# Kernel tuning notes

Hardware: AMD Instinct MI355X
Metric: run time of the kernel (lower is better)

The kernel has to match this reference:

```python
import jax, jax.numpy as jnp
import numpy as np

N = 50000      # nodes
E = 800000     # edges
D_IN, D_HID, D_OUT = 1433, 64, 7
EPS = 1e-7       # eps[float32] in hgcn Hyperboloid
MIN_NORM = 1e-15
MAX_NORM = 1e6
# c = 1 -> K = 1/c = 1, sqrtK = 1 (folded into constants below)


def proj(x):
    # reset time coordinate so point lies on the hyperboloid
    y = x[:, 1:]
    y_sqnorm = jnp.sum(y * y, axis=1, keepdims=True)
    x0 = jnp.sqrt(jnp.clip(1.0 + y_sqnorm, EPS))
    return jnp.concatenate([x0, y], axis=1)


def proj_tan0(u):
    return jnp.concatenate([jnp.zeros_like(u[:, :1]), u[:, 1:]], axis=1)


def expmap0(u):
    x = u[:, 1:]
    x_norm = jnp.clip(jnp.linalg.norm(x, axis=1, keepdims=True), MIN_NORM)
    theta = x_norm
    res = jnp.concatenate([jnp.cosh(theta), jnp.sinh(theta) * x / x_norm], axis=1)
    return proj(res)


def logmap0(x):
    y = x[:, 1:]
    y_norm = jnp.clip(jnp.linalg.norm(y, axis=1, keepdims=True), MIN_NORM)
    theta = jnp.clip(x[:, :1], 1.0 + EPS)
    return jnp.concatenate([jnp.zeros_like(theta), jnp.arccosh(theta) * y / y_norm], axis=1)


def minkowski_dot(x, y):
    return jnp.sum(x * y, axis=-1, keepdims=True) - 2.0 * x[:, :1] * y[:, :1]


def proj_tan(u, x):
    ux = jnp.sum(x[:, 1:] * u[:, 1:], axis=1, keepdims=True)
    v0 = ux / jnp.clip(x[:, :1], EPS)
    return jnp.concatenate([v0, u[:, 1:]], axis=1)


def expmap(u, x):
    normu = jnp.sqrt(jnp.clip(minkowski_dot(u, u), EPS))
    normu = jnp.minimum(normu, MAX_NORM)
    theta = jnp.clip(normu, MIN_NORM)
    result = jnp.cosh(theta) * x + jnp.sinh(theta) * u / theta
    return proj(result)


def ptransp0(x, u):
    x0, y = x[:, :1], x[:, 1:]
    y_norm = jnp.clip(jnp.linalg.norm(y, axis=1, keepdims=True), MIN_NORM)
    yn = y / y_norm
    v = jnp.concatenate([-y_norm, (1.0 - x0) * yn], axis=1)
    alpha = jnp.sum(yn * u[:, 1:], axis=1, keepdims=True)
    return proj_tan(u - alpha * v, x)


def mobius_add(x, y):
    u = logmap0(y)
    v = ptransp0(x, u)
    return expmap(v, x)


def hyp_linear(x, W, b):
    # mobius_matvec then hyperbolic bias add (dropout=0)
    mv = expmap0(logmap0(x) @ W.T)
    res = proj(mv)
    hyp_bias = proj(expmap0(proj_tan0(b[None, :])))
    return proj(mobius_add(res, hyp_bias))


def hyp_agg(x, row, col, edge_weight):
    # spmm(adj, logmap0(x)) via edge-list scatter-add
    xt = logmap0(x)
    msg = edge_weight[:, None] * xt[col]          # [E, d]
    support = jax.ops.segment_sum(msg, row, num_segments=N)
    return proj(expmap0(support))


def hyp_act(x):
    xt = jax.nn.relu(logmap0(x))
    xt = proj_tan0(xt)
    return proj(expmap0(xt))


def setup_inputs() -> dict:
    key = jax.random.key(0)
    ks = jax.random.split(key, 8)
    return {
        "x": jax.random.normal(ks[0], (N, D_IN), dtype=jnp.float32),
        "row": jax.random.randint(ks[1], (E,), 0, N),
        "col": jax.random.randint(ks[2], (E,), 0, N),
        "edge_weight": jax.random.uniform(ks[3], (E,), dtype=jnp.float32) * 0.1,
        "W1": jax.random.normal(ks[4], (D_HID, D_IN), dtype=jnp.float32) * 0.02,
        "b1": jax.random.normal(ks[5], (D_HID,), dtype=jnp.float32) * 0.02,
        "W2": jax.random.normal(ks[6], (D_OUT, D_HID), dtype=jnp.float32) * 0.05,
        "b2": jax.random.normal(ks[7], (D_OUT,), dtype=jnp.float32) * 0.02,
    }


def reference(x, row, col, edge_weight, W1, b1, W2, b2):
    # map features to the hyperboloid
    x_hyp = proj(expmap0(proj_tan0(x)))
    # layer 1: HypLinear -> HypAgg -> HypAct
    h = hyp_act(hyp_agg(hyp_linear(x_hyp, W1, b1), row, col, edge_weight))
    # layer 2
    h = hyp_act(hyp_agg(hyp_linear(h, W2, b2), row, col, edge_weight))
    # back to tangent space at origin
    return proj_tan0(logmap0(h))
```

## Files before the change

kernel.cpp:

```cpp
#include <hip/hip_runtime.h>
#include <hip/hip_bf16.h>

#define NN 50000
#define EE 800000
#define DIN 1433
#define KTOT 1432
#define KHALF 716
#define NKT 23
#define NB 196
#define EPSC 1e-7f
#define MINN 1e-15f
#define MAXN 1e6f

typedef __attribute__((ext_vector_type(8))) short bf16x8;
typedef __attribute__((ext_vector_type(4))) float f32x4;

#define WF_OFF     0
#define Z1A_OFF    94208
#define Z1B_OFF    (Z1A_OFF + 3200000)
#define XTB_OFF    (Z1B_OFF + 3200000)
#define XT3_OFF    (XTB_OFF + 1600000)
#define CNT_OFF    (XT3_OFF + 400000)
#define ROWPTR_OFF (CNT_OFF + 50000)
#define CUR_OFF    (ROWPTR_OFF + 50002)
#define BSUM_OFF   (CUR_OFF + 50000)
#define UB_OFF     (BSUM_OFF + 256)
#define EP_OFF     (UB_OFF + 128)

__device__ __forceinline__ float wsum(float v) {
#pragma unroll
  for (int o = 1; o < 64; o <<= 1) v += __shfl_xor(v, o, 64);
  return v;
}

__device__ __forceinline__ float gsum8(float v) {
#pragma unroll
  for (int o = 1; o < 8; o <<= 1) v += __shfl_xor(v, o, 64);
  return v;
}

__device__ __forceinline__ void split_bf(float v, unsigned int& hbits16, unsigned int& lbits16) {
  unsigned int b = __float_as_uint(v);
  unsigned int hb = b & 0xFFFF0000u;
  float r = v - __uint_as_float(hb);
  unsigned int lb = __float_as_uint(r);
  lbits16 = (lb + 0x7FFFu + ((lb >> 16) & 1u)) >> 16;
  hbits16 = hb >> 16;
}

__device__ __forceinline__ unsigned short f2bf_rne(float v) {
  unsigned int b = __float_as_uint(v);
  return (unsigned short)((b + 0x7FFFu + ((b >> 16) & 1u)) >> 16);
}
__device__ __forceinline__ float bf2f(unsigned short u) {
  return __uint_as_float(((unsigned int)u) << 16);
}

__device__ __forceinline__ float fsinh(float x) {
  float e = __expf(x);
  return 0.5f * (e - __fdividef(1.f, e));
}
__device__ __forceinline__ float facoshp(float z) {
  return __logf(z + sqrtf(fmaxf(z * z - 1.f, 0.f)));
}

__device__ float bias_tangent(const float* b, int lane, int D) {
  const bool sp = (lane >= 1) && (lane < D);
  float bsp = sp ? b[lane] : 0.f;
  float rb = fmaxf(sqrtf(wsum(bsp * bsp)), MINN);
  float bsh = fsinh(rb);
  float hb = sp ? bsh * __fdividef(bsp, rb) : 0.f;
  float hbn2 = wsum(hb * hb);
  float hb0 = sqrtf(fmaxf(1.f + hbn2, EPSC));
  float hbyn = fmaxf(sqrtf(hbn2), MINN);
  return sp ? facoshp(fmaxf(hb0, 1.f + EPSC)) * __fdividef(hb, hbyn) : 0.f;
}

__device__ float chain_with_u(float z, float u, int lane, int D) {
  const bool sp = (lane >= 1) && (lane < D);
  float s = sp ? z : 0.f;
  float r = fmaxf(sqrtf(wsum(s * s)), MINN);
  float sh = fsinh(r);
  float y = sp ? sh * __fdividef(s, r) : 0.f;
  float yn2 = wsum(y * y);
  float x0 = sqrtf(fmaxf(1.f + yn2, EPSC));
  float y_norm = fmaxf(sqrtf(yn2), MINN);
  float ynv = sp ? __fdividef(y, y_norm) : 0.f;
  float alpha = wsum(ynv * u);
  float wsp = sp ? u - alpha * (1.f - x0) * ynv : 0.f;
  float ux = wsum(y * wsp);
  float v0 = __fdividef(ux, fmaxf(x0, EPSC));
  float vt = (lane == 0) ? v0 : wsp;
  float md = wsum(vt * vt) - 2.f * v0 * v0;
  float nu = sqrtf(fmaxf(md, EPSC));
  nu = fminf(nu, MAXN);
  float th = fmaxf(nu, MINN);
  float e = __expf(th), ei = __fdividef(1.f, e);
  float cth = 0.5f * (e + ei), sth = 0.5f * (e - ei);
  float resx = (lane == 0) ? x0 : y;
  float eres = fmaf(cth, resx, sth * __fdividef(vt, th));
  float en2 = wsum(sp ? eres * eres : 0.f);
  float e0 = sqrtf(fmaxf(1.f + en2, EPSC));
  float eyn = fmaxf(sqrtf(en2), MINN);
  return sp ? facoshp(fmaxf(e0, 1.f + EPSC)) * __fdividef(eres, eyn) : 0.f;
}

__device__ float agg_act_chain(float sin_, int lane, int D) {
  const bool sp = (lane >= 1) && (lane < D);
  float s = sp ? sin_ : 0.f;
  float r = fmaxf(sqrtf(wsum(s * s)), MINN);
  float sh = fsinh(r);
  float g = sp ? sh * __fdividef(s, r) : 0.f;
  float gn2 = wsum(g * g);
  float g0 = sqrtf(fmaxf(1.f + gn2, EPSC));
  float gyn = fmaxf(sqrtf(gn2), MINN);
  float l = sp ? facoshp(fmaxf(g0, 1.f + EPSC)) * __fdividef(g, gyn) : 0.f;
  float t = fmaxf(l, 0.f);
  float rt = fmaxf(sqrtf(wsum(t * t)), MINN);
  float sht = fsinh(rt);
  float h = sp ? sht * __fdividef(t, rt) : 0.f;
  float hn2 = wsum(h * h);
  float h0 = sqrtf(fmaxf(1.f + hn2, EPSC));
  float hyn = fmaxf(sqrtf(hn2), MINN);
  return sp ? facoshp(fmaxf(h0, 1.f + EPSC)) * __fdividef(h, hyn) : 0.f;
}

__device__ float agg_act_chain8(float sin_, int f) {
  const bool sp = (f >= 1) && (f < 7);
  float s = sp ? sin_ : 0.f;
  float r = fmaxf(sqrtf(gsum8(s * s)), MINN);
  float sh = fsinh(r);
  float g = sp ? sh * __fdividef(s, r) : 0.f;
  float gn2 = gsum8(g * g);
  float g0 = sqrtf(fmaxf(1.f + gn2, EPSC));
  float gyn = fmaxf(sqrtf(gn2), MINN);
  float l = sp ? facoshp(fmaxf(g0, 1.f + EPSC)) * __fdividef(g, gyn) : 0.f;
  float t = fmaxf(l, 0.f);
  float rt = fmaxf(sqrtf(gsum8(t * t)), MINN);
  float sht = fsinh(rt);
  float h = sp ? sht * __fdividef(t, rt) : 0.f;
  float hn2 = gsum8(h * h);
  float h0 = sqrtf(fmaxf(1.f + hn2, EPSC));
  float hyn = fmaxf(sqrtf(hn2), MINN);
  return sp ? facoshp(fmaxf(h0, 1.f + EPSC)) * __fdividef(h, hyn) : 0.f;
}

__global__ __launch_bounds__(256) void prep_wb_zero(const float* __restrict__ W1,
                                                    const float* __restrict__ b1,
                                                    const float* __restrict__ b2,
                                                    unsigned short* __restrict__ wfrag,
                                                    float* __restrict__ ub,
                                                    int* __restrict__ cnt) {
  if (blockIdx.x >= 93) {
    int i = (blockIdx.x - 93) * 256 + threadIdx.x;
    if (i < NN) cnt[i] = 0;
    return;
  }
  if (blockIdx.x == 92) {
    const int w = threadIdx.x >> 6, lane = threadIdx.x & 63;
    if (w == 0) ub[lane] = bias_tangent(b1, lane, 64);
    else if (w == 1) ub[64 + lane] = bias_tangent(b2, lane, 7);
    return;
  }
  int idx = blockIdx.x * 256 + threadIdx.x;
  int lane = idx & 63;
  int c = (idx >> 6) & 7;
  int rest = idx >> 9;
  int kt = rest % NKT;
  int half = rest / NKT;
  int type = c >> 2, nt = c & 3;
  int col = nt * 16 + (lane & 15);
  unsigned short vals[8];
#pragma unroll
  for (int i = 0; i < 8; ++i) {
    int lk = kt * 32 + (lane >> 4) * 8 + i;
    float wv = (lk < KHALF) ? W1[col * DIN + half * KHALF + lk + 1] : 0.f;
    unsigned int h16, l16;
    split_bf(wv, h16, l16);
    vals[i] = (unsigned short)((type == 0) ? h16 : l16);
  }
  unsigned short* dst = wfrag + (((size_t)(half * NKT + kt) * 8 + c) * 64 + lane) * 8;
#pragma unroll
  for (int i = 0; i < 8; ++i) dst[i] = vals[i];
}

__global__ __launch_bounds__(256) void k_blocksum(const int* __restrict__ cnt,
                                                  int* __restrict__ bsum) {
  __shared__ int wpart[4];
  int i = blockIdx.x * 256 + threadIdx.x;
  int v = (i < NN) ? cnt[i] : 0;
  int s = v;
#pragma unroll
  for (int o = 1; o < 64; o <<= 1) s += __shfl_xor(s, o, 64);
  if ((threadIdx.x & 63) == 0) wpart[threadIdx.x >> 6] = s;
  __syncthreads();
  if (threadIdx.x == 0) bsum[blockIdx.x] = wpart[0] + wpart[1] + wpart[2] + wpart[3];
}

__global__ __launch_bounds__(256) void k_scan_apply(const int* __restrict__ cnt,
                                                    const int* __restrict__ bsum,
                                                    int* __restrict__ rowptr,
                                                    int* __restrict__ cur) {
  __shared__ int s[256];
  __shared__ int base_sh;
  const int t = threadIdx.x;
  const int b = blockIdx.x;
  int bv = (t < NB) ? bsum[t] : 0;
  s[t] = bv;
  __syncthreads();
  for (int o = 1; o < 256; o <<= 1) {
    int a = (t >= o) ? s[t - o] : 0;
    __syncthreads();
    s[t] += a;
    __syncthreads();
  }
  if (t == b) base_sh = s[b] - bv;
  __syncthreads();
  const int base = base_sh;
  __syncthreads();
  int i = b * 256 + t;
  int v = (i < NN) ? cnt[i] : 0;
  s[t] = v;
  __syncthreads();
  for (int o = 1; o < 256; o <<= 1) {
    int a = (t >= o) ? s[t - o] : 0;
    __syncthreads();
    s[t] += a;
    __syncthreads();
  }
  int ex = s[t] - v + base;
  if (i < NN) { rowptr[i] = ex; cur[i] = ex; }
  if (i == NN - 1) rowptr[NN] = EE;
}

__global__ __launch_bounds__(256) void gemm_hist(const float* __restrict__ x,
                                                 const unsigned short* __restrict__ wfrag,
                                                 float* __restrict__ z,
                                                 const int* __restrict__ row,
                                                 int* __restrict__ cnt) {
  if (blockIdx.y == 2) {
    int e = blockIdx.x * 512 + threadIdx.x;
    if (e < EE) atomicAdd(&cnt[row[e]], 1);
    e += 256;
    if (e < EE) atomicAdd(&cnt[row[e]], 1);
    return;
  }
  __shared__ __align__(16) float XA[3 * 1024];
  __shared__ __align__(16) unsigned short BB[2][8][64][8];
  const int tid = threadIdx.x;
  const int w = tid >> 6, lane = tid & 63;
  const int row0 = blockIdx.x * 32;
  const int half = blockIdx.y;
  const unsigned short* wf = wfrag + (size_t)half * NKT * 4096;
  float* zp = z + (size_t)half * 3200000;
  const int nt0 = (w >> 1) * 2;

  auto stageB = [&](int kt, int p) {
    const unsigned short* src = wf + (size_t)kt * 4096 + (2 * w) * 512 + lane * 8;
    __builtin_amdgcn_global_load_lds(
        (const __attribute__((address_space(1))) unsigned int*)src,
        (__attribute__((address_space(3))) unsigned int*)(&BB[p][2 * w][0][0]), 16, 0, 0);
    __builtin_amdgcn_global_load_lds(
        (const __attribute__((address_space(1))) unsigned int*)(src + 512),
        (__attribute__((address_space(3))) unsigned int*)(&BB[p][2 * w + 1][0][0]), 16, 0, 0);
  };
  auto stageA = [&](int kt, int q) {
    const int r = w * 8 + (lane >> 3);
    const int lb = (lane & 7) ^ (r & 7);
    int grow = row0 + r; if (grow >= NN) grow = NN - 1;
    size_t off = (size_t)grow * DIN + 1 + half * KHALF + kt * 32 + lb * 4;
    if (off > (size_t)NN * DIN - 4) off = (size_t)NN * DIN - 4;
    __builtin_amdgcn_global_load_lds(
        (const __attribute__((address_space(1))) unsigned int*)(x + off),
        (__attribute__((address_space(3))) unsigned int*)(XA + q * 1024 + w * 256),
        16, 0, 0);
  };

  f32x4 acc[2];
  acc[0] = (f32x4){0.f, 0.f, 0.f, 0.f};
  acc[1] = (f32x4){0.f, 0.f, 0.f, 0.f};

  stageB(0, 0);
  stageA(0, 0);
  stageA(1, 1);
  __builtin_amdgcn_sched_barrier(0);
  asm volatile("s_waitcnt vmcnt(1)" ::: "memory");
  __builtin_amdgcn_s_barrier();
  __builtin_amdgcn_sched_barrier(0);

  const int rr = (w & 1) * 16 + (lane & 15);
  const int b0 = (lane >> 4) * 2;
  const int pb0 = (b0 ^ (rr & 7)) * 4;
  const int pb1 = ((b0 + 1) ^ (rr & 7)) * 4;

  for (int kt = 0; kt < NKT; ++kt) {
    if (kt + 1 < NKT) stageB(kt + 1, (kt + 1) & 1);
    if (kt + 2 < NKT) stageA(kt + 2, (kt + 2) % 3);
    const float* xa = XA + (kt % 3) * 1024 + rr * 32;
    float4 f0 = *(const float4*)(xa + pb0);
    float4 f1 = *(const float4*)(xa + pb1);
    float af[8] = {f0.x, f0.y, f0.z, f0.w, f1.x, f1.y, f1.z, f1.w};
    unsigned int h[8], l[8];
#pragma unroll
    for (int j = 0; j < 8; ++j) split_bf(af[j], h[j], l[j]);
    bf16x8 ah, al;
#pragma unroll
    for (int j = 0; j < 8; ++j) { ah[j] = (short)h[j]; al[j] = (short)l[j]; }
    bf16x8 bh[2], bl[2];
#pragma unroll
    for (int n = 0; n < 2; ++n) {
      bh[n] = *(const bf16x8*)&BB[kt & 1][nt0 + n][lane][0];
      bl[n] = *(const bf16x8*)&BB[kt & 1][4 + nt0 + n][lane][0];
    }
    __builtin_amdgcn_s_setprio(1);
#pragma unroll
    for (int n = 0; n < 2; ++n) {
      acc[n] = __builtin_amdgcn_mfma_f32_16x16x32_bf16(ah, bh[n], acc[n], 0, 0, 0);
      acc[n] = __builtin_amdgcn_mfma_f32_16x16x32_bf16(ah, bl[n], acc[n], 0, 0, 0);
      acc[n] = __builtin_amdgcn_mfma_f32_16x16x32_bf16(al, bh[n], acc[n], 0, 0, 0);
    }
    __builtin_amdgcn_s_setprio(0);
    if (kt + 1 < NKT) {
      __builtin_amdgcn_sched_barrier(0);
      asm volatile("s_waitcnt lgkmcnt(0)" ::: "memory");
      if (kt + 2 < NKT) asm volatile("s_waitcnt vmcnt(1)" ::: "memory");
      else              asm volatile("s_waitcnt vmcnt(0)" ::: "memory");
      __builtin_amdgcn_s_barrier();
      __builtin_amdgcn_sched_barrier(0);
    }
  }
#pragma unroll
  for (int n = 0; n < 2; ++n)
#pragma unroll
    for (int i = 0; i < 4; ++i) {
      int orow = row0 + (w & 1) * 16 + (lane >> 4) * 4 + i;
      int ocol = (nt0 + n) * 16 + (lane & 15);
      if (orow < NN) zp[(size_t)orow * 64 + ocol] = acc[n][i];
    }
}

__global__ __launch_bounds__(256) void node1_scatter(const float* __restrict__ z1a,
                                                     const float* __restrict__ z1b,
                                                     const float* __restrict__ ub,
                                                     unsigned short* __restrict__ xtb,
                                                     const int* __restrict__ row,
                                                     const int* __restrict__ col,
                                                     const float* __restrict__ ew,
                                                     int* __restrict__ cur,
                                                     uint2* __restrict__ ep) {
  if (blockIdx.x >= 12500) {
    int e = (blockIdx.x - 12500) * 256 + threadIdx.x;
    if (e < EE) {
      int p = atomicAdd(&cur[row[e]], 1);
      uint2 q;
      q.x = (unsigned int)col[e];
      q.y = __float_as_uint(ew[e]);
      ep[p] = q;
    }
    return;
  }
  const int node = blockIdx.x * 4 + (threadIdx.x >> 6);
  const int lane = threadIdx.x & 63;
  const int idx = node * 64 + lane;
  float z = z1a[idx] + z1b[idx];
  float u1 = ub[lane];
  float o = chain_with_u(z, u1, lane, 64);
  xtb[idx] = f2bf_rne(o);
}

__global__ __launch_bounds__(256) void agg1_node2(const int* __restrict__ rowptr,
                                                  const uint2* __restrict__ ep,
                                                  const unsigned short* __restrict__ xtb,
                                                  const float* __restrict__ W2,
                                                  const float* __restrict__ ub,
                                                  float* __restrict__ xt3) {
  const int node = blockIdx.x * 4 + (threadIdx.x >> 6);
  const int lane = threadIdx.x & 63;
  const int s0 = rowptr[node], s1 = rowptr[node + 1];
  float a0 = 0.f, a1 = 0.f, a2 = 0.f, a3 = 0.f;
  float a4 = 0.f, a5 = 0.f, a6 = 0.f, a7 = 0.f;
  for (int p = s0; p < s1; p += 8) {
    int p1 = min(p + 1, s1 - 1), p2 = min(p + 2, s1 - 1), p3 = min(p + 3, s1 - 1);
    int p4 = min(p + 4, s1 - 1), p5 = min(p + 5, s1 - 1), p6 = min(p + 6, s1 - 1), p7 = min(p + 7, s1 - 1);
    uint2 q0 = ep[p], q1 = ep[p1], q2 = ep[p2], q3 = ep[p3];
    uint2 q4 = ep[p4], q5 = ep[p5], q6 = ep[p6], q7 = ep[p7];
    float w0 = __uint_as_float(q0.y);
    float w1 = (p + 1 < s1) ? __uint_as_float(q1.y) : 0.f;
    float w2 = (p + 2 < s1) ? __uint_as_float(q2.y) : 0.f;
    float w3 = (p + 3 < s1) ? __uint_as_float(q3.y) : 0.f;
    float w4 = (p + 4 < s1) ? __uint_as_float(q4.y) : 0.f;
    float w5 = (p + 5 < s1) ? __uint_as_float(q5.y) : 0.f;
    float w6 = (p + 6 < s1) ? __uint_as_float(q6.y) : 0.f;
    float w7 = (p + 7 < s1) ? __uint_as_float(q7.y) : 0.f;
    a0 = fmaf(w0, bf2f(xtb[(size_t)q0.x * 64 + lane]), a0);
    a1 = fmaf(w1, bf2f(xtb[(size_t)q1.x * 64 + lane]), a1);
    a2 = fmaf(w2, bf2f(xtb[(size_t)q2.x * 64 + lane]), a2);
    a3 = fmaf(w3, bf2f(xtb[(size_t)q3.x * 64 + lane]), a3);
    a4 = fmaf(w4, bf2f(xtb[(size_t)q4.x * 64 + lane]), a4);
    a5 = fmaf(w5, bf2f(xtb[(size_t)q5.x * 64 + lane]), a5);
    a6 = fmaf(w6, bf2f(xtb[(size_t)q6.x * 64 + lane]), a6);
    a7 = fmaf(w7, bf2f(xtb[(size_t)q7.x * 64 + lane]), a7);
  }
  float acc = ((a0 + a1) + (a2 + a3)) + ((a4 + a5) + (a6 + a7));
  float xt2 = agg_act_chain(acc, lane, 64);
  float z2 = 0.f;
#pragma unroll
  for (int jj = 1; jj < 7; ++jj) {
    float wv = W2[jj * 64 + lane];
    float sjj = wsum(xt2 * wv);
    if (lane == jj) z2 = sjj;
  }
  float u2 = ub[64 + lane];
  float o = chain_with_u(z2, u2, lane, 7);
  if (lane < 8) xt3[node * 8 + lane] = o;
}

__global__ __launch_bounds__(256) void agg2_final(const int* __restrict__ rowptr,
                                                  const uint2* __restrict__ ep,
                                                  const float* __restrict__ xt3,
                                                  float* __restrict__ out) {
  const int node = blockIdx.x * 32 + (threadIdx.x >> 3);
  const int f = threadIdx.x & 7;
  const int nc = (node < NN) ? node : (NN - 1);
  const int s0 = rowptr[nc], s1 = rowptr[nc + 1];
  float a0 = 0.f, a1 = 0.f, a2 = 0.f, a3 = 0.f;
  for (int p = s0; p < s1; p += 4) {
    int p1 = min(p + 1, s1 - 1), p2 = min(p + 2, s1 - 1), p3 = min(p + 3, s1 - 1);
    uint2 q0 = ep[p], q1 = ep[p1], q2 = ep[p2], q3 = ep[p3];
    float w0 = __uint_as_float(q0.y);
    float w1 = (p + 1 < s1) ? __uint_as_float(q1.y) : 0.f;
    float w2 = (p + 2 < s1) ? __uint_as_float(q2.y) : 0.f;
    float w3 = (p + 3 < s1) ? __uint_as_float(q3.y) : 0.f;
    a0 = fmaf(w0, xt3[(size_t)q0.x * 8 + f], a0);
    a1 = fmaf(w1, xt3[(size_t)q1.x * 8 + f], a1);
    a2 = fmaf(w2, xt3[(size_t)q2.x * 8 + f], a2);
    a3 = fmaf(w3, xt3[(size_t)q3.x * 8 + f], a3);
  }
  float acc = (a0 + a1) + (a2 + a3);
  float o = agg_act_chain8(acc, f);
  if (node < NN && f < 7) out[node * 7 + f] = o;
}

extern "C" void kernel_launch(void* const* d_in, const int* in_sizes, int n_in,
                              void* d_out, int out_size, void* d_ws, size_t ws_size,
                              hipStream_t stream) {
  const float* x = (const float*)d_in[0];
  const int* row = (const int*)d_in[1];
  const int* col = (const int*)d_in[2];
  const float* ew = (const float*)d_in[3];
  const float* W1 = (const float*)d_in[4];
  const float* b1 = (const float*)d_in[5];
  const float* W2 = (const float*)d_in[6];
  const float* b2 = (const float*)d_in[7];
  float* ws = (float*)d_ws;
  unsigned short* wfrag = (unsigned short*)(ws + WF_OFF);
  float* z1a = ws + Z1A_OFF;
  float* z1b = ws + Z1B_OFF;
  unsigned short* xtb = (unsigned short*)(ws + XTB_OFF);
  float* xt3 = ws + XT3_OFF;
  int* cnt = (int*)(ws + CNT_OFF);
  int* rowptr = (int*)(ws + ROWPTR_OFF);
  int* cur = (int*)(ws + CUR_OFF);
  int* bsum = (int*)(ws + BSUM_OFF);
  float* ub = ws + UB_OFF;
  uint2* ep = (uint2*)(ws + EP_OFF);
  float* out = (float*)d_out;

  prep_wb_zero<<<dim3(289), dim3(256), 0, stream>>>(W1, b1, b2, wfrag, ub, cnt);

  gemm_hist<<<dim3(1563, 3), dim3(256), 0, stream>>>(x, wfrag, z1a, row, cnt);

  k_blocksum<<<dim3(NB), dim3(256), 0, stream>>>(cnt, bsum);
  k_scan_apply<<<dim3(NB), dim3(256), 0, stream>>>(cnt, bsum, rowptr, cur);

  node1_scatter<<<dim3(15625), dim3(256), 0, stream>>>(z1a, z1b, ub, xtb,
                                                       row, col, ew, cur, ep);

  agg1_node2<<<dim3(12500), dim3(256), 0, stream>>>(rowptr, ep, xtb, W2, ub, xt3);
  agg2_final<<<dim3(1563), dim3(256), 0, stream>>>(rowptr, ep, xt3, out);
}
```

Baseline: 282.8 us.

## Double GEMM row tile to 64 rows per block for B-fragment reuse

Each gemm_hist block now computes 64 rows instead of 32, with each wave running two M sub-tiles against the same staged W fragments. The grid halves, and the histogram blocks now process four edges per thread to match. The aim is to reuse each B tile load and barrier across twice the MFMA work and to cut per-block overhead. In exchange it uses more LDS and registers per block, and fewer blocks may leave occupancy lower for this memory-bound x stream.

```diff
diff --git a/kernel.cpp b/kernel.cpp
--- a/kernel.cpp
+++ b/kernel.cpp
@@ -239,17 +239,19 @@
                                                  const int* __restrict__ row,
                                                  int* __restrict__ cnt) {
   if (blockIdx.y == 2) {
-    int e = blockIdx.x * 512 + threadIdx.x;
-    if (e < EE) atomicAdd(&cnt[row[e]], 1);
-    e += 256;
-    if (e < EE) atomicAdd(&cnt[row[e]], 1);
+    int e = blockIdx.x * 1024 + threadIdx.x;
+#pragma unroll
+    for (int i = 0; i < 4; ++i) {
+      if (e < EE) atomicAdd(&cnt[row[e]], 1);
+      e += 256;
+    }
     return;
   }
-  __shared__ __align__(16) float XA[3 * 1024];
+  __shared__ __align__(16) float XA[3 * 2048];
   __shared__ __align__(16) unsigned short BB[2][8][64][8];
   const int tid = threadIdx.x;
   const int w = tid >> 6, lane = tid & 63;
-  const int row0 = blockIdx.x * 32;
+  const int row0 = blockIdx.x * 64;
   const int half = blockIdx.y;
   const unsigned short* wf = wfrag + (size_t)half * NKT * 4096;
   float* zp = z + (size_t)half * 3200000;
@@ -265,47 +267,55 @@
         (__attribute__((address_space(3))) unsigned int*)(&BB[p][2 * w + 1][0][0]), 16, 0, 0);
   };
   auto stageA = [&](int kt, int q) {
-    const int r = w * 8 + (lane >> 3);
-    const int lb = (lane & 7) ^ (r & 7);
-    int grow = row0 + r; if (grow >= NN) grow = NN - 1;
-    size_t off = (size_t)grow * DIN + 1 + half * KHALF + kt * 32 + lb * 4;
-    if (off > (size_t)NN * DIN - 4) off = (size_t)NN * DIN - 4;
-    __builtin_amdgcn_global_load_lds(
-        (const __attribute__((address_space(1))) unsigned int*)(x + off),
-        (__attribute__((address_space(3))) unsigned int*)(XA + q * 1024 + w * 256),
-        16, 0, 0);
+#pragma unroll
+    for (int i = 0; i < 2; ++i) {
+      const int r = w * 16 + i * 8 + (lane >> 3);
+      const int lb = (lane & 7) ^ (r & 7);
+      int grow = row0 + r; if (grow >= NN) grow = NN - 1;
+      size_t off = (size_t)grow * DIN + 1 + half * KHALF + kt * 32 + lb * 4;
+      if (off > (size_t)NN * DIN - 4) off = (size_t)NN * DIN - 4;
+      __builtin_amdgcn_global_load_lds(
+          (const __attribute__((address_space(1))) unsigned int*)(x + off),
+          (__attribute__((address_space(3))) unsigned int*)(XA + q * 2048 + w * 512 + i * 256),
+          16, 0, 0);
+    }
   };
 
-  f32x4 acc[2];
-  acc[0] = (f32x4){0.f, 0.f, 0.f, 0.f};
-  acc[1] = (f32x4){0.f, 0.f, 0.f, 0.f};
+  f32x4 acc[2][2];
+#pragma unroll
+  for (int m = 0; m < 2; ++m)
+#pragma unroll
+    for (int n = 0; n < 2; ++n) acc[m][n] = (f32x4){0.f, 0.f, 0.f, 0.f};
 
   stageB(0, 0);
   stageA(0, 0);
   stageA(1, 1);
   __builtin_amdgcn_sched_barrier(0);
-  asm volatile("s_waitcnt vmcnt(1)" ::: "memory");
+  asm volatile("s_waitcnt vmcnt(2)" ::: "memory");
   __builtin_amdgcn_s_barrier();
   __builtin_amdgcn_sched_barrier(0);
 
-  const int rr = (w & 1) * 16 + (lane & 15);
+  const int rrb = (w & 1) * 32 + (lane & 15);
   const int b0 = (lane >> 4) * 2;
-  const int pb0 = (b0 ^ (rr & 7)) * 4;
-  const int pb1 = ((b0 + 1) ^ (rr & 7)) * 4;
 
   for (int kt = 0; kt < NKT; ++kt) {
     if (kt + 1 < NKT) stageB(kt + 1, (kt + 1) & 1);
     if (kt + 2 < NKT) stageA(kt + 2, (kt + 2) % 3);
-    const float* xa = XA + (kt % 3) * 1024 + rr * 32;
-    float4 f0 = *(const float4*)(xa + pb0);
-    float4 f1 = *(const float4*)(xa + pb1);
-    float af[8] = {f0.x, f0.y, f0.z, f0.w, f1.x, f1.y, f1.z, f1.w};
-    unsigned int h[8], l[8];
-#pragma unroll
-    for (int j = 0; j < 8; ++j) split_bf(af[j], h[j], l[j]);
-    bf16x8 ah, al;
-#pragma unroll
-    for (int j = 0; j < 8; ++j) { ah[j] = (short)h[j]; al[j] = (short)l[j]; }
+    const float* xaq = XA + (kt % 3) * 2048;
+    bf16x8 ah[2], al[2];
+#pragma unroll
+    for (int m = 0; m < 2; ++m) {
+      const int rr = rrb + m * 16;
+      const float* xa = xaq + rr * 32;
+      float4 f0 = *(const float4*)(xa + ((b0 ^ (rr & 7)) * 4));
+      float4 f1 = *(const float4*)(xa + (((b0 + 1) ^ (rr & 7)) * 4));
+      float af[8] = {f0.x, f0.y, f0.z, f0.w, f1.x, f1.y, f1.z, f1.w};
+      unsigned int h[8], l[8];
+#pragma unroll
+      for (int j = 0; j < 8; ++j) split_bf(af[j], h[j], l[j]);
+#pragma unroll
+      for (int j = 0; j < 8; ++j) { ah[m][j] = (short)h[j]; al[m][j] = (short)l[j]; }
+    }
     bf16x8 bh[2], bl[2];
 #pragma unroll
     for (int n = 0; n < 2; ++n) {
@@ -314,29 +324,33 @@
     }
     __builtin_amdgcn_s_setprio(1);
 #pragma unroll
-    for (int n = 0; n < 2; ++n) {
-      acc[n] = __builtin_amdgcn_mfma_f32_16x16x32_bf16(ah, bh[n], acc[n], 0, 0, 0);
-      acc[n] = __builtin_amdgcn_mfma_f32_16x16x32_bf16(ah, bl[n], acc[n], 0, 0, 0);
-      acc[n] = __builtin_amdgcn_mfma_f32_16x16x32_bf16(al, bh[n], acc[n], 0, 0, 0);
-    }
+    for (int m = 0; m < 2; ++m)
+#pragma unroll
+      for (int n = 0; n < 2; ++n) {
+        acc[m][n] = __builtin_amdgcn_mfma_f32_16x16x32_bf16(ah[m], bh[n], acc[m][n], 0, 0, 0);
+        acc[m][n] = __builtin_amdgcn_mfma_f32_16x16x32_bf16(ah[m], bl[n], acc[m][n], 0, 0, 0);
+        acc[m][n] = __builtin_amdgcn_mfma_f32_16x16x32_bf16(al[m], bh[n], acc[m][n], 0, 0, 0);
+      }
     __builtin_amdgcn_s_setprio(0);
     if (kt + 1 < NKT) {
       __builtin_amdgcn_sched_barrier(0);
       asm volatile("s_waitcnt lgkmcnt(0)" ::: "memory");
-      if (kt + 2 < NKT) asm volatile("s_waitcnt vmcnt(1)" ::: "memory");
+      if (kt + 2 < NKT) asm volatile("s_waitcnt vmcnt(2)" ::: "memory");
       else              asm volatile("s_waitcnt vmcnt(0)" ::: "memory");
       __builtin_amdgcn_s_barrier();
       __builtin_amdgcn_sched_barrier(0);
     }
   }
 #pragma unroll
-  for (int n = 0; n < 2; ++n)
-#pragma unroll
-    for (int i = 0; i < 4; ++i) {
-      int orow = row0 + (w & 1) * 16 + (lane >> 4) * 4 + i;
-      int ocol = (nt0 + n) * 16 + (lane & 15);
-      if (orow < NN) zp[(size_t)orow * 64 + ocol] = acc[n][i];
-    }
+  for (int m = 0; m < 2; ++m)
+#pragma unroll
+    for (int n = 0; n < 2; ++n)
+#pragma unroll
+      for (int i = 0; i < 4; ++i) {
+        int orow = row0 + (w & 1) * 32 + m * 16 + (lane >> 4) * 4 + i;
+        int ocol = (nt0 + n) * 16 + (lane & 15);
+        if (orow < NN) zp[(size_t)orow * 64 + ocol] = acc[m][n][i];
+      }
 }
 
 __global__ __launch_bounds__(256) void node1_scatter(const float* __restrict__ z1a,
@@ -468,7 +482,7 @@
 
   prep_wb_zero<<<dim3(289), dim3(256), 0, stream>>>(W1, b1, b2, wfrag, ub, cnt);
 
-  gemm_hist<<<dim3(1563, 3), dim3(256), 0, stream>>>(x, wfrag, z1a, row, cnt);
+  gemm_hist<<<dim3(782, 3), dim3(256), 0, stream>>>(x, wfrag, z1a, row, cnt);
 
   k_blocksum<<<dim3(NB), dim3(256), 0, stream>>>(cnt, bsum);
   k_scan_apply<<<dim3(NB), dim3(256), 0, stream>>>(cnt, bsum, rowptr, cur);
```

Measured after the change: 268.7 us. 5.0% less time.
